# Kernel tuning notes

Measured on AMD Instinct MI355X. Metric: run time of the kernel, lower is better.

The kernel has to match this reference:

```python
import jax, jax.numpy as jnp
import numpy as np

D = 4096      # input_size == hidden_size (required by the broadcast add in the update)
T = 8192      # sequence length
F = 10        # num_factor (hard-coded in the module)
OUT = 10      # output_size
BETA = 0.1    # exponential scale for decay factors


def setup_inputs() -> dict:
    key = jax.random.key(0)
    ks = jax.random.split(key, 4)
    inp = jax.random.normal(ks[0], (T, 1, D), dtype=jnp.float32)
    hidden = jnp.zeros((1, F, D), dtype=jnp.float32)
    # decay factors: 1 - clip(Exp(beta), 0, 1-eps), each broadcast across hidden dim
    rng = np.random.default_rng(0)
    d = 1.0 - np.clip(rng.exponential(BETA, F), 0.0, 1.0 - np.finfo(np.float32).eps)
    w = jnp.broadcast_to(jnp.asarray(d, jnp.float32)[None, :, None], (1, F, D))
    pool_w = jax.random.normal(ks[1], (1, F, 1), jnp.float32) * (1.0 / np.sqrt(F))
    pool_b = jnp.zeros((1,), jnp.float32)
    H1 = (D + D) // 2  # (input_size + hidden_size) // 2
    i2o_w = jax.random.normal(ks[2], (H1, 2 * D), jnp.float32) * (1.0 / np.sqrt(2 * D))
    i2o_b = jnp.zeros((H1,), jnp.float32)
    o_w = jax.random.normal(ks[3], (OUT, H1), jnp.float32) * (1.0 / np.sqrt(H1))
    o_b = jnp.zeros((OUT,), jnp.float32)
    return dict(inp=inp, hidden=hidden, w=w, pool_w=pool_w, pool_b=pool_b,
                i2o_w=i2o_w, i2o_b=i2o_b, o_w=o_w, o_b=o_b)


def reference(inp, hidden, w, pool_w, pool_b, i2o_w, i2o_b, o_w, o_b):
    # inp: [T, 1, D]; hidden: [1, F, D] decay-state
    Tn = inp.shape[0]

    def step(carry, xt):
        h, hsum = carry
        hsum = hsum + h                   # pre-update hidden feeds the pooled feature
        h_new = w * h + xt[:, None, :]    # decay-weighted update, x broadcast over factors
        return (h_new, hsum), None

    (h_final, h_sum), _ = jax.lax.scan(step, (hidden, jnp.zeros_like(hidden)), inp)

    # Conv1d(F, 1, 1) pooling is linear -> sum over time of pool(h_t) = pool(sum_t h_t)
    pooled_sum = jnp.einsum('f,bfd->bd', pool_w[0, :, 0], h_sum) + Tn * pool_b  # [1, D]
    x_sum = inp.sum(axis=0)  # [1, D]

    # avg_feature at the last step = cumulative sum of combined / steps
    avg = jnp.concatenate([x_sum, pooled_sum], axis=1) / Tn  # [1, 2D]
    pred = jax.nn.relu(avg @ i2o_w.T + i2o_b) @ o_w.T + o_b  # [1, OUT]
    return pred, h_final
```

## Files before the change

### kernel.cpp

```cpp
#include <hip/hip_runtime.h>

#define TLEN 8192
#define DD   4096
#define NF   10
#define NC   12
#define NACC 12

__device__ __forceinline__ double powi_d(double w, int n) {
    double a = 1.0, p = w;
    while (n) { if (n & 1) a *= p; p *= p; n >>= 1; }
    return a;
}

__global__ void coef_kernel(const float* __restrict__ w,
                            const float* __restrict__ pool_w,
                            float* __restrict__ coef) {
    int t = blockIdx.x * blockDim.x + threadIdx.x;
    if (t >= TLEN) return;
    int n = TLEN - 1 - t;
    double g = 0.0;
#pragma unroll
    for (int f = 0; f < NF; ++f) {
        double wf = (double)w[(size_t)f * DD];
        double a  = powi_d(wf, n);
        double den = 1.0 - wf;
        double c  = (den > 1e-30) ? (1.0 - a) / den : (double)n;
        g += (double)pool_w[f] * c;
        coef[t * NC + f] = (float)a;
    }
    coef[t * NC + NF]     = (float)g;
    coef[t * NC + NF + 1] = 0.0f;
}

__global__ __launch_bounds__(256) void pass_kernel(const float* __restrict__ inp,
                                                   const float* __restrict__ coef,
                                                   float* __restrict__ part,
                                                   int rows) {
    __shared__ float sc[256 * NC];
    const int t0 = blockIdx.y * rows;
    const int d  = blockIdx.x * 1024 + threadIdx.x * 4;

    float sx=0,sy=0,sz=0,sw=0;
    float px=0,py=0,pz=0,pw4=0;
    float hx[NF], hy[NF], hz[NF], hw[NF];
#pragma unroll
    for (int f = 0; f < NF; ++f) { hx[f]=0; hy[f]=0; hz[f]=0; hw[f]=0; }

    const float* ip = inp + (size_t)t0 * DD + d;

    for (int rbase = 0; rbase < rows; rbase += 256) {
        int rcnt = rows - rbase; if (rcnt > 256) rcnt = 256;
        __syncthreads();
        for (int i = threadIdx.x; i < rcnt * NC; i += 256)
            sc[i] = coef[(size_t)(t0 + rbase) * NC + i];
        __syncthreads();
        for (int r = 0; r < rcnt; ++r) {
            float4 x = *(const float4*)ip;
            ip += DD;
            const float* cf = &sc[r * NC];
            sx += x.x; sy += x.y; sz += x.z; sw += x.w;
            float g = cf[NF];
            px  = fmaf(g, x.x, px);  py  = fmaf(g, x.y, py);
            pz  = fmaf(g, x.z, pz);  pw4 = fmaf(g, x.w, pw4);
#pragma unroll
            for (int f = 0; f < NF; ++f) {
                float a = cf[f];
                hx[f] = fmaf(a, x.x, hx[f]); hy[f] = fmaf(a, x.y, hy[f]);
                hz[f] = fmaf(a, x.z, hz[f]); hw[f] = fmaf(a, x.w, hw[f]);
            }
        }
    }

    size_t base = ((size_t)blockIdx.y * NC) * DD + d;
    *(float4*)(part + base)      = make_float4(sx, sy, sz, sw);
    *(float4*)(part + base + DD) = make_float4(px, py, pz, pw4);
#pragma unroll
    for (int f = 0; f < NF; ++f)
        *(float4*)(part + base + (size_t)(2 + f) * DD) =
            make_float4(hx[f], hy[f], hz[f], hw[f]);
}

__global__ void reduce_kernel(const float* __restrict__ part,
                              float* __restrict__ red, int C) {
    int idx = blockIdx.x * blockDim.x + threadIdx.x;
    if (idx >= NACC * DD) return;
    float s = 0.0f;
    for (int c = 0; c < C; ++c)
        s += part[(size_t)c * NC * DD + idx];
    red[idx] = s;
}

__global__ void finalize_kernel(const float* __restrict__ red,
                                const float* __restrict__ w,
                                const float* __restrict__ pool_w,
                                const float* __restrict__ pool_b,
                                const float* __restrict__ hidden,
                                float* __restrict__ out,
                                float* __restrict__ avg) {
    int i = blockIdx.x * blockDim.x + threadIdx.x;
    int d = i * 4;
    float4 xs = *(const float4*)(red + d);
    float4 pl = *(const float4*)(red + DD + d);
    const float invT = 1.0f / (float)TLEN;
#pragma unroll
    for (int f = 0; f < NF; ++f) {
        double wf = (double)w[(size_t)f * DD];
        double wTd = powi_d(wf, TLEN);
        double den = 1.0 - wf;
        double sTd = (den > 1e-30) ? (1.0 - wTd) / den : (double)TLEN;
        float wT = (float)wTd;
        float pwsT = (float)((double)pool_w[f] * sTd);
        float4 hf = *(const float4*)(red + (size_t)(2 + f) * DD + d);
        float4 h0 = *(const float4*)(hidden + (size_t)f * DD + d);
        hf.x = fmaf(wT, h0.x, hf.x); hf.y = fmaf(wT, h0.y, hf.y);
        hf.z = fmaf(wT, h0.z, hf.z); hf.w = fmaf(wT, h0.w, hf.w);
        pl.x = fmaf(pwsT, h0.x, pl.x); pl.y = fmaf(pwsT, h0.y, pl.y);
        pl.z = fmaf(pwsT, h0.z, pl.z); pl.w = fmaf(pwsT, h0.w, pl.w);
        float* o = out + 10 + (size_t)f * DD + d;
        o[0] = hf.x; o[1] = hf.y; o[2] = hf.z; o[3] = hf.w;
    }
    float pb = pool_b[0];
    avg[d+0] = xs.x * invT; avg[d+1] = xs.y * invT;
    avg[d+2] = xs.z * invT; avg[d+3] = xs.w * invT;
    avg[DD + d + 0] = pl.x * invT + pb; avg[DD + d + 1] = pl.y * invT + pb;
    avg[DD + d + 2] = pl.z * invT + pb; avg[DD + d + 3] = pl.w * invT + pb;
}

__global__ __launch_bounds__(256) void gemv_kernel(const float* __restrict__ W,
                                                   const float* __restrict__ b,
                                                   const float* __restrict__ avg,
                                                   float* __restrict__ hid) {
    int row  = blockIdx.x * 4 + (threadIdx.x >> 6);
    int lane = threadIdx.x & 63;
    const float* wr = W + (size_t)row * (2 * DD);
    float acc = 0.0f;
#pragma unroll 8
    for (int j0 = 0; j0 < 32; ++j0) {
        int j = j0 * 256 + lane * 4;
        float4 wv = *(const float4*)(wr + j);
        float4 av = *(const float4*)(avg + j);
        acc = fmaf(wv.x, av.x, acc); acc = fmaf(wv.y, av.y, acc);
        acc = fmaf(wv.z, av.z, acc); acc = fmaf(wv.w, av.w, acc);
    }
    for (int off = 32; off; off >>= 1) acc += __shfl_down(acc, off, 64);
    if (lane == 0) hid[row] = fmaxf(acc + b[row], 0.0f);
}

__global__ void out_kernel(const float* __restrict__ hid,
                           const float* __restrict__ ow,
                           const float* __restrict__ ob,
                           float* __restrict__ out) {
    __shared__ float redl[256];
    int o = blockIdx.x;
    float acc = 0.0f;
    for (int h = threadIdx.x; h < DD; h += 256)
        acc = fmaf(hid[h], ow[(size_t)o * DD + h], acc);
    redl[threadIdx.x] = acc;
    __syncthreads();
    for (int s = 128; s; s >>= 1) {
        if (threadIdx.x < s) redl[threadIdx.x] += redl[threadIdx.x + s];
        __syncthreads();
    }
    if (threadIdx.x == 0) out[o] = redl[0] + ob[o];
}

extern "C" void kernel_launch(void* const* d_in, const int* in_sizes, int n_in,
                              void* d_out, int out_size, void* d_ws, size_t ws_size,
                              hipStream_t stream) {
    const float* inp    = (const float*)d_in[0];
    const float* hidden = (const float*)d_in[1];
    const float* w      = (const float*)d_in[2];
    const float* pw     = (const float*)d_in[3];
    const float* pb     = (const float*)d_in[4];
    const float* i2o_w  = (const float*)d_in[5];
    const float* i2o_b  = (const float*)d_in[6];
    const float* o_w    = (const float*)d_in[7];
    const float* o_b    = (const float*)d_in[8];
    float* out = (float*)d_out;
    float* ws  = (float*)d_ws;

    float* coef = ws;
    float* red  = ws + 98304;
    float* avg  = ws + 147456;
    float* hid  = ws + 155648;
    float* part = ws + 159744;

    int C = 128;
    while (C > 1) {
        size_t need = (159744 + (size_t)C * NC * DD) * sizeof(float);
        if (need <= ws_size) break;
        C >>= 1;
    }
    int rows = TLEN / C;

    coef_kernel<<<TLEN / 256, 256, 0, stream>>>(w, pw, coef);
    pass_kernel<<<dim3(4, C), 256, 0, stream>>>(inp, coef, part, rows);
    reduce_kernel<<<(NACC * DD + 255) / 256, 256, 0, stream>>>(part, red, C);
    finalize_kernel<<<4, 256, 0, stream>>>(red, w, pw, pb, hidden, out, avg);
    gemv_kernel<<<DD / 4, 256, 0, stream>>>(i2o_w, i2o_b, avg, hid);
    out_kernel<<<10, 256, 0, stream>>>(hid, o_w, o_b, out);
}
```

Baseline: 113.4 us.

## Fuse coefficient computation into pass kernel and merge reduce with finalize

Each pass block now computes its own decay powers and pooled coefficients in shared memory, which removes the separate coef kernel. The chunk-partials reduction and the finalize step are merged into one widely parallel kernel that applies the initial-hidden corrections per element. The chunk count is now fixed at 128 rather than sized to the workspace. Together this cuts two launches and a global round trip, at the cost of recomputing double-precision powers in every block.

After: 115.4 us. No clear change (+1.7%).

```diff
diff --git a/kernel.cpp b/kernel.cpp
--- a/kernel.cpp
+++ b/kernel.cpp
@@ -5,6 +5,8 @@
 #define NF   10
 #define NC   12
 #define NACC 12
+#define CCH  128
+#define ROWS 64
 
 __device__ __forceinline__ double powi_d(double w, int n) {
     double a = 1.0, p = w;
@@ -12,34 +14,35 @@
     return a;
 }
 
-__global__ void coef_kernel(const float* __restrict__ w,
-                            const float* __restrict__ pool_w,
-                            float* __restrict__ coef) {
-    int t = blockIdx.x * blockDim.x + threadIdx.x;
-    if (t >= TLEN) return;
-    int n = TLEN - 1 - t;
-    double g = 0.0;
+__global__ __launch_bounds__(256) void pass_kernel(const float* __restrict__ inp,
+                                                   const float* __restrict__ w,
+                                                   const float* __restrict__ pool_w,
+                                                   float* __restrict__ part) {
+    __shared__ float sc [ROWS * NC];
+    __shared__ float scg[ROWS * NF];
+    const int ch = blockIdx.y;
+    const int t0 = ch * ROWS;
+
+    for (int i = threadIdx.x; i < ROWS * NF; i += 256) {
+        int r = i / NF, f = i - r * NF;
+        double wf = (double)w[(size_t)f * DD];
+        int n = TLEN - 1 - (t0 + r);
+        double a = powi_d(wf, n);
+        double den = 1.0 - wf;
+        sc[r * NC + f] = (float)a;
+        scg[i] = (float)((den > 1e-30) ? (double)pool_w[f] * (1.0 - a) / den
+                                       : (double)pool_w[f] * (double)n);
+    }
+    __syncthreads();
+    if (threadIdx.x < ROWS) {
+        float g = 0.0f;
 #pragma unroll
-    for (int f = 0; f < NF; ++f) {
-        double wf = (double)w[(size_t)f * DD];
-        double a  = powi_d(wf, n);
-        double den = 1.0 - wf;
-        double c  = (den > 1e-30) ? (1.0 - a) / den : (double)n;
-        g += (double)pool_w[f] * c;
-        coef[t * NC + f] = (float)a;
+        for (int f = 0; f < NF; ++f) g += scg[threadIdx.x * NF + f];
+        sc[threadIdx.x * NC + NF] = g;
     }
-    coef[t * NC + NF]     = (float)g;
-    coef[t * NC + NF + 1] = 0.0f;
-}
+    __syncthreads();
 
-__global__ __launch_bounds__(256) void pass_kernel(const float* __restrict__ inp,
-                                                   const float* __restrict__ coef,
-                                                   float* __restrict__ part,
-                                                   int rows) {
-    __shared__ float sc[256 * NC];
-    const int t0 = blockIdx.y * rows;
-    const int d  = blockIdx.x * 1024 + threadIdx.x * 4;
-
+    const int d = blockIdx.x * 1024 + threadIdx.x * 4;
     float sx=0,sy=0,sz=0,sw=0;
     float px=0,py=0,pz=0,pw4=0;
     float hx[NF], hy[NF], hz[NF], hw[NF];
@@ -47,31 +50,23 @@
     for (int f = 0; f < NF; ++f) { hx[f]=0; hy[f]=0; hz[f]=0; hw[f]=0; }
 
     const float* ip = inp + (size_t)t0 * DD + d;
-
-    for (int rbase = 0; rbase < rows; rbase += 256) {
-        int rcnt = rows - rbase; if (rcnt > 256) rcnt = 256;
-        __syncthreads();
-        for (int i = threadIdx.x; i < rcnt * NC; i += 256)
-            sc[i] = coef[(size_t)(t0 + rbase) * NC + i];
-        __syncthreads();
-        for (int r = 0; r < rcnt; ++r) {
-            float4 x = *(const float4*)ip;
-            ip += DD;
-            const float* cf = &sc[r * NC];
-            sx += x.x; sy += x.y; sz += x.z; sw += x.w;
-            float g = cf[NF];
-            px  = fmaf(g, x.x, px);  py  = fmaf(g, x.y, py);
-            pz  = fmaf(g, x.z, pz);  pw4 = fmaf(g, x.w, pw4);
+    for (int r = 0; r < ROWS; ++r) {
+        float4 x = *(const float4*)ip;
+        ip += DD;
+        const float* cf = &sc[r * NC];
+        sx += x.x; sy += x.y; sz += x.z; sw += x.w;
+        float g = cf[NF];
+        px  = fmaf(g, x.x, px);  py  = fmaf(g, x.y, py);
+        pz  = fmaf(g, x.z, pz);  pw4 = fmaf(g, x.w, pw4);
 #pragma unroll
-            for (int f = 0; f < NF; ++f) {
-                float a = cf[f];
-                hx[f] = fmaf(a, x.x, hx[f]); hy[f] = fmaf(a, x.y, hy[f]);
-                hz[f] = fmaf(a, x.z, hz[f]); hw[f] = fmaf(a, x.w, hw[f]);
-            }
+        for (int f = 0; f < NF; ++f) {
+            float a = cf[f];
+            hx[f] = fmaf(a, x.x, hx[f]); hy[f] = fmaf(a, x.y, hy[f]);
+            hz[f] = fmaf(a, x.z, hz[f]); hw[f] = fmaf(a, x.w, hw[f]);
         }
     }
 
-    size_t base = ((size_t)blockIdx.y * NC) * DD + d;
+    size_t base = ((size_t)ch * NACC) * DD + d;
     *(float4*)(part + base)      = make_float4(sx, sy, sz, sw);
     *(float4*)(part + base + DD) = make_float4(px, py, pz, pw4);
 #pragma unroll
@@ -80,50 +75,56 @@
             make_float4(hx[f], hy[f], hz[f], hw[f]);
 }
 
-__global__ void reduce_kernel(const float* __restrict__ part,
-                              float* __restrict__ red, int C) {
-    int idx = blockIdx.x * blockDim.x + threadIdx.x;
-    if (idx >= NACC * DD) return;
-    float s = 0.0f;
-    for (int c = 0; c < C; ++c)
-        s += part[(size_t)c * NC * DD + idx];
-    red[idx] = s;
-}
-
-__global__ void finalize_kernel(const float* __restrict__ red,
-                                const float* __restrict__ w,
-                                const float* __restrict__ pool_w,
-                                const float* __restrict__ pool_b,
-                                const float* __restrict__ hidden,
-                                float* __restrict__ out,
-                                float* __restrict__ avg) {
-    int i = blockIdx.x * blockDim.x + threadIdx.x;
-    int d = i * 4;
-    float4 xs = *(const float4*)(red + d);
-    float4 pl = *(const float4*)(red + DD + d);
-    const float invT = 1.0f / (float)TLEN;
-#pragma unroll
-    for (int f = 0; f < NF; ++f) {
+__global__ __launch_bounds__(256) void redfin_kernel(const float* __restrict__ part,
+                                                     const float* __restrict__ w,
+                                                     const float* __restrict__ pool_w,
+                                                     const float* __restrict__ pool_b,
+                                                     const float* __restrict__ hidden,
+                                                     float* __restrict__ out,
+                                                     float* __restrict__ avg) {
+    __shared__ float swT[NF], spwsT[NF];
+    if (threadIdx.x < NF) {
+        int f = threadIdx.x;
         double wf = (double)w[(size_t)f * DD];
         double wTd = powi_d(wf, TLEN);
         double den = 1.0 - wf;
         double sTd = (den > 1e-30) ? (1.0 - wTd) / den : (double)TLEN;
-        float wT = (float)wTd;
-        float pwsT = (float)((double)pool_w[f] * sTd);
-        float4 hf = *(const float4*)(red + (size_t)(2 + f) * DD + d);
-        float4 h0 = *(const float4*)(hidden + (size_t)f * DD + d);
-        hf.x = fmaf(wT, h0.x, hf.x); hf.y = fmaf(wT, h0.y, hf.y);
-        hf.z = fmaf(wT, h0.z, hf.z); hf.w = fmaf(wT, h0.w, hf.w);
-        pl.x = fmaf(pwsT, h0.x, pl.x); pl.y = fmaf(pwsT, h0.y, pl.y);
-        pl.z = fmaf(pwsT, h0.z, pl.z); pl.w = fmaf(pwsT, h0.w, pl.w);
-        float* o = out + 10 + (size_t)f * DD + d;
-        o[0] = hf.x; o[1] = hf.y; o[2] = hf.z; o[3] = hf.w;
+        swT[f]   = (float)wTd;
+        spwsT[f] = (float)((double)pool_w[f] * sTd);
     }
-    float pb = pool_b[0];
-    avg[d+0] = xs.x * invT; avg[d+1] = xs.y * invT;
-    avg[d+2] = xs.z * invT; avg[d+3] = xs.w * invT;
-    avg[DD + d + 0] = pl.x * invT + pb; avg[DD + d + 1] = pl.y * invT + pb;
-    avg[DD + d + 2] = pl.z * invT + pb; avg[DD + d + 3] = pl.w * invT + pb;
+    __syncthreads();
+
+    const int idx = blockIdx.x * 256 + threadIdx.x;
+    const int acc = idx >> 12;
+    const int d   = idx & (DD - 1);
+
+    float s0=0,s1=0,s2=0,s3=0,s4=0,s5=0,s6=0,s7=0;
+#pragma unroll
+    for (int c = 0; c < CCH; c += 8) {
+        s0 += part[(size_t)(c+0) * (NACC*DD) + idx];
+        s1 += part[(size_t)(c+1) * (NACC*DD) + idx];
+        s2 += part[(size_t)(c+2) * (NACC*DD) + idx];
+        s3 += part[(size_t)(c+3) * (NACC*DD) + idx];
+        s4 += part[(size_t)(c+4) * (NACC*DD) + idx];
+        s5 += part[(size_t)(c+5) * (NACC*DD) + idx];
+        s6 += part[(size_t)(c+6) * (NACC*DD) + idx];
+        s7 += part[(size_t)(c+7) * (NACC*DD) + idx];
+    }
+    float s = ((s0+s1)+(s2+s3)) + ((s4+s5)+(s6+s7));
+
+    const float invT = 1.0f / (float)TLEN;
+    if (acc == 0) {
+        avg[d] = s * invT;
+    } else if (acc == 1) {
+        float corr = 0.0f;
+#pragma unroll
+        for (int f = 0; f < NF; ++f)
+            corr = fmaf(spwsT[f], hidden[(size_t)f * DD + d], corr);
+        avg[DD + d] = (s + corr) * invT + pool_b[0];
+    } else {
+        int f = acc - 2;
+        out[10 + (size_t)f * DD + d] = fmaf(swT[f], hidden[(size_t)f * DD + d], s);
+    }
 }
 
 __global__ __launch_bounds__(256) void gemv_kernel(const float* __restrict__ W,
@@ -179,24 +180,12 @@
     float* out = (float*)d_out;
     float* ws  = (float*)d_ws;
 
-    float* coef = ws;
-    float* red  = ws + 98304;
-    float* avg  = ws + 147456;
-    float* hid  = ws + 155648;
-    float* part = ws + 159744;
+    float* avg  = ws;
+    float* hid  = ws + 8192;
+    float* part = ws + 12288;
 
-    int C = 128;
-    while (C > 1) {
-        size_t need = (159744 + (size_t)C * NC * DD) * sizeof(float);
-        if (need <= ws_size) break;
-        C >>= 1;
-    }
-    int rows = TLEN / C;
-
-    coef_kernel<<<TLEN / 256, 256, 0, stream>>>(w, pw, coef);
-    pass_kernel<<<dim3(4, C), 256, 0, stream>>>(inp, coef, part, rows);
-    reduce_kernel<<<(NACC * DD + 255) / 256, 256, 0, stream>>>(part, red, C);
-    finalize_kernel<<<4, 256, 0, stream>>>(red, w, pw, pb, hidden, out, avg);
-    gemv_kernel<<<DD / 4, 256, 0, stream>>>(i2o_w, i2o_b, avg, hid);
-    out_kernel<<<10, 256, 0, stream>>>(hid, o_w, o_b, out);
+    pass_kernel  <<<dim3(4, CCH), 256, 0, stream>>>(inp, w, pw, part);
+    redfin_kernel<<<192, 256, 0, stream>>>(part, w, pw, pb, hidden, out, avg);
+    gemv_kernel  <<<DD / 4, 256, 0, stream>>>(i2o_w, i2o_b, avg, hid);
+    out_kernel   <<<10, 256, 0, stream>>>(hid, o_w, o_b, out);
 }
```
